# Performance work log

Measured on AMD Instinct MI355X. Metric: run time of the kernel, lower is better.

Reference implementation:

```python
import jax, jax.numpy as jnp
import numpy as np


def conv2d(x, w, b, pad):
    # x: [B,Cin,H,W], w: [Cout,Cin,kh,kw]
    y = jax.lax.conv_general_dilated(
        x, w, window_strides=(1, 1), padding=[(pad, pad), (pad, pad)],
        dimension_numbers=('NCHW', 'OIHW', 'NCHW'))
    return y + b[None, :, None, None]


def setup_inputs() -> dict:
    key = jax.random.key(0)
    ks = jax.random.split(key, 11)
    B, C, H, W = 4, 128, 64, 64
    Cc, Hc, Wc = 256, 32, 32
    s = 0.05
    return {
        'sr_feat': jax.random.normal(ks[0], (B, C, H, W), jnp.float32),
        'context_feat': jax.random.normal(ks[1], (B, Cc, Hc, Wc), jnp.float32),
        'Wq': jax.random.normal(ks[2], (C, C, 1, 1), jnp.float32) * s,
        'bq': jax.random.normal(ks[3], (C,), jnp.float32) * s,
        'Wk': jax.random.normal(ks[4], (C, Cc, 1, 1), jnp.float32) * s,
        'bk': jax.random.normal(ks[5], (C,), jnp.float32) * s,
        'Wv': jax.random.normal(ks[6], (C, Cc, 1, 1), jnp.float32) * s,
        'bv': jax.random.normal(ks[7], (C,), jnp.float32) * s,
        'Wp': jax.random.normal(ks[8], (C, C, 3, 3), jnp.float32) * s,
        'bp': jax.random.normal(ks[9], (C,), jnp.float32) * s,
        'gamma': jax.random.normal(ks[10], (1,), jnp.float32) * s,
    }


def reference(sr_feat, context_feat, Wq, bq, Wk, bk, Wv, bv, Wp, bp, gamma):
    B, C, H, W = sr_feat.shape
    Cc = context_feat.shape[1]
    # bilinear upsample (half-pixel centers == align_corners=False)
    ctx = jax.image.resize(context_feat, (B, Cc, H, W), method='bilinear')
    q = conv2d(sr_feat, Wq, bq, 0).reshape(B, C, H * W)   # [B,C,N]
    k = conv2d(ctx, Wk, bk, 0).reshape(B, C, H * W)       # [B,C,N]
    v = conv2d(ctx, Wv, bv, 0).reshape(B, C, H * W)       # [B,C,N]
    # attn[b,n,m] = softmax_m( sum_c q[b,c,n] * k[b,c,m] )
    attn = jax.nn.softmax(jnp.einsum('bcn,bcm->bnm', q, k), axis=-1)
    # out[b,c,n] = sum_m v[b,c,m] * attn[b,n,m]
    out = jnp.einsum('bcm,bnm->bcn', v, attn).reshape(B, C, H, W)
    return sr_feat + gamma[0] * conv2d(out, Wp, bp, 1)
```

## Files before the change

### kernel.cpp

```cpp
#include <hip/hip_runtime.h>
#include <math.h>

#define NB 4
#define C  128
#define CCH 256
#define HH 64
#define WW 64
#define NN 4096
#define NS 1024
#define HC 32
#define WC 32
#define PP 66
#define LOG2E 1.44269504088896f
#define NSPLIT 4

typedef unsigned short u16;
typedef unsigned int uint32;
typedef short s16x8 __attribute__((ext_vector_type(8)));
typedef float f32x4 __attribute__((ext_vector_type(4)));
typedef float f32x16 __attribute__((ext_vector_type(16)));

#if __has_builtin(__builtin_amdgcn_exp2f)
#define EXP2(x) __builtin_amdgcn_exp2f(x)
#else
#define EXP2(x) __expf((x) * 0.69314718056f)
#endif

__device__ __forceinline__ u16 f2bf(float f) {
    uint32 u = __float_as_uint(f);
    u += 0x7fffu + ((u >> 16) & 1u);
    return (u16)(u >> 16);
}
__device__ __forceinline__ float bf2f(u16 h) {
    return __uint_as_float((uint32)h << 16);
}

__global__ __launch_bounds__(256) void prep2(const float* __restrict__ ctx,
                                             const float* __restrict__ sr,
                                             const float* __restrict__ Wq,
                                             const float* __restrict__ Wk,
                                             const float* __restrict__ Wv,
                                             const float* __restrict__ Wp,
                                             u16* __restrict__ ctx_s,
                                             u16* __restrict__ sr_t,
                                             u16* __restrict__ wbf,
                                             u16* __restrict__ wt,
                                             uint4* __restrict__ att_z) {
    __shared__ float ls[64 * 65];
    int blk = blockIdx.x;
    int tid = threadIdx.x;

    if (blk < 256) {
        int idx = blk;
        int n0 = (idx & 15) * 64;
        int ci0 = ((idx >> 4) & 3) * 64;
        int b = idx >> 6;
        const float* inb = ctx + ((size_t)b * CCH + ci0) * NS + n0;
#pragma unroll
        for (int L = 0; L < 4; L++) {
            int fc = tid + L * 256;
            int nc = fc & 15, ci = fc >> 4;
            float4 v = *(const float4*)(inb + (size_t)ci * NS + nc * 4);
            float* d = &ls[ci * 65 + nc * 4];
            d[0] = v.x; d[1] = v.y; d[2] = v.z; d[3] = v.w;
        }
        __syncthreads();
        u16* ob = ctx_s + ((size_t)b * NS + n0) * CCH + ci0;
#pragma unroll
        for (int j = 0; j < 16; j++) {
            int o = tid + j * 256;
            int ci = o & 63, n = o >> 6;
            ob[(size_t)n * CCH + ci] = f2bf(ls[ci * 65 + n]);
        }
    } else if (blk < 768) {
        int idx = blk - 256;
        int n0 = (idx & 63) * 64;
        int ci0 = ((idx >> 6) & 1) * 64;
        int b = idx >> 7;
        const float* inb = sr + ((size_t)b * C + ci0) * NN + n0;
#pragma unroll
        for (int L = 0; L < 4; L++) {
            int fc = tid + L * 256;
            int nc = fc & 15, ci = fc >> 4;
            float4 v = *(const float4*)(inb + (size_t)ci * NN + nc * 4);
            float* d = &ls[ci * 65 + nc * 4];
            d[0] = v.x; d[1] = v.y; d[2] = v.z; d[3] = v.w;
        }
        __syncthreads();
        u16* ob = sr_t + ((size_t)b * NN + n0) * C + ci0;
#pragma unroll
        for (int j = 0; j < 16; j++) {
            int o = tid + j * 256;
            int ci = o & 63, n = o >> 6;
            ob[(size_t)n * C + ci] = f2bf(ls[ci * 65 + n]);
        }
    } else if (blk < 1664) {
        int i = (blk - 768) * 256 + tid;
        if (i < 81920) {
            float v;
            if (i < 16384) v = Wq[i] * LOG2E;
            else if (i < 49152) v = Wk[i - 16384];
            else v = Wv[i - 49152];
            wbf[i] = f2bf(v);
        } else {
            int idx = i - 81920;
            int ciin = idx & 31;
            int co = (idx >> 5) & 127;
            int cb = (idx >> 12) & 3;
            int pos = idx >> 14;
            int ky = pos / 3, kx = pos - ky * 3;
            int ci = cb * 32 + ciin;
            wt[idx] = f2bf(Wp[((size_t)(co * C + ci) * 3 + ky) * 3 + kx]);
        }
    } else {
        int i = (blk - 1664) * 256 + tid;
        if (i < 278784) att_z[i] = make_uint4(0, 0, 0, 0);
    }
}

__global__ __launch_bounds__(256) void proj_all2(const u16* __restrict__ sr_t,
                                                 const u16* __restrict__ ctx_s,
                                                 const u16* __restrict__ wbf,
                                                 const float* __restrict__ bq,
                                                 const float* __restrict__ bk,
                                                 const float* __restrict__ bv,
                                                 u16* __restrict__ q_t,
                                                 u16* __restrict__ k_s,
                                                 u16* __restrict__ v_s) {
    __shared__ u16 xs[128 * 64];
    __shared__ u16 wsm[2][128 * 64];
    int b = blockIdx.y;
    int tid = threadIdx.x;
    int w = tid >> 6, lane = tid & 63, l31 = lane & 31, half = lane >> 5;
    int xh = w >> 1, wh = w & 1;

    if (blockIdx.x < 32) {
        int n0 = blockIdx.x * 128;
        const u16* xb = sr_t + (size_t)b * NN * C;
        f32x16 acc[2][2];
#pragma unroll
        for (int xt = 0; xt < 2; xt++)
#pragma unroll
            for (int wt2 = 0; wt2 < 2; wt2++)
#pragma unroll
                for (int i = 0; i < 16; i++) acc[xt][wt2][i] = 0.f;
        for (int c0i = 0; c0i < 2; c0i++) {
            int c0 = c0i * 64;
            __syncthreads();
#pragma unroll
            for (int t = 0; t < 4; t++) {
                int CI = t * 256 + tid;
                int row = CI >> 3, sl = CI & 7;
                int lc = sl ^ (row & 7);
                __builtin_amdgcn_global_load_lds(
                    (const __attribute__((address_space(1))) void*)(xb + (size_t)(n0 + row) * C + c0 + lc * 8),
                    (__attribute__((address_space(3))) void*)&xs[(size_t)CI * 8], 16, 0, 0);
            }
#pragma unroll
            for (int t = 0; t < 4; t++) {
                int CI = t * 256 + tid;
                int co = CI >> 3, sl = CI & 7;
                int lc = sl ^ (co & 7);
                __builtin_amdgcn_global_load_lds(
                    (const __attribute__((address_space(1))) void*)(wbf + (size_t)co * C + c0 + lc * 8),
                    (__attribute__((address_space(3))) void*)&wsm[0][(size_t)CI * 8], 16, 0, 0);
            }
            __syncthreads();
#pragma unroll
            for (int kg = 0; kg < 4; kg++) {
                int pc = ((kg * 2 + half) ^ (l31 & 7)) * 8;
                s16x8 xf[2], wf2[2];
#pragma unroll
                for (int xt = 0; xt < 2; xt++)
                    xf[xt] = *(const s16x8*)&xs[(xh * 64 + xt * 32 + l31) * 64 + pc];
#pragma unroll
                for (int wt2 = 0; wt2 < 2; wt2++)
                    wf2[wt2] = *(const s16x8*)&wsm[0][(wh * 64 + wt2 * 32 + l31) * 64 + pc];
#pragma unroll
                for (int xt = 0; xt < 2; xt++)
#pragma unroll
                    for (int wt2 = 0; wt2 < 2; wt2++)
                        acc[xt][wt2] = __builtin_amdgcn_mfma_f32_32x32x16_bf16(xf[xt], wf2[wt2], acc[xt][wt2], 0, 0, 0);
            }
        }
        u16* ot = q_t + (size_t)b * NN * C;
        float bv2[2];
#pragma unroll
        for (int wt2 = 0; wt2 < 2; wt2++) bv2[wt2] = bq[wh * 64 + wt2 * 32 + l31] * LOG2E;
#pragma unroll
        for (int xt = 0; xt < 2; xt++)
#pragma unroll
            for (int r = 0; r < 16; r++) {
                int n = n0 + xh * 64 + xt * 32 + (r & 3) + 8 * (r >> 2) + 4 * half;
#pragma unroll
                for (int wt2 = 0; wt2 < 2; wt2++)
                    ot[(size_t)n * C + wh * 64 + wt2 * 32 + l31] = f2bf(acc[xt][wt2][r] + bv2[wt2]);
            }
    } else {
        int n0 = (blockIdx.x - 32) * 64;
        const u16* xb = ctx_s + (size_t)b * NS * CCH;
        const u16* wkb = wbf + 16384;
        const u16* wvb = wbf + 49152;
        f32x16 acck[2], accv[2];
#pragma unroll
        for (int wt2 = 0; wt2 < 2; wt2++)
#pragma unroll
            for (int i = 0; i < 16; i++) { acck[wt2][i] = 0.f; accv[wt2][i] = 0.f; }
        for (int c0i = 0; c0i < 4; c0i++) {
            int c0 = c0i * 64;
            __syncthreads();
#pragma unroll
            for (int t = 0; t < 2; t++) {
                int CI = t * 256 + tid;
                int row = CI >> 3, sl = CI & 7;
                int lc = sl ^ (row & 7);
                __builtin_amdgcn_global_load_lds(
                    (const __attribute__((address_space(1))) void*)(xb + (size_t)(n0 + row) * CCH + c0 + lc * 8),
                    (__attribute__((address_space(3))) void*)&xs[(size_t)CI * 8], 16, 0, 0);
            }
#pragma unroll
            for (int t = 0; t < 4; t++) {
                int CI = t * 256 + tid;
                int co = CI >> 3, sl = CI & 7;
                int lc = sl ^ (co & 7);
                __builtin_amdgcn_global_load_lds(
                    (const __attribute__((address_space(1))) void*)(wkb + (size_t)co * CCH + c0 + lc * 8),
                    (__attribute__((address_space(3))) void*)&wsm[0][(size_t)CI * 8], 16, 0, 0);
            }
#pragma unroll
            for (int t = 0; t < 4; t++) {
                int CI = t * 256 + tid;
                int co = CI >> 3, sl = CI & 7;
                int lc = sl ^ (co & 7);
                __builtin_amdgcn_global_load_lds(
                    (const __attribute__((address_space(1))) void*)(wvb + (size_t)co * CCH + c0 + lc * 8),
                    (__attribute__((address_space(3))) void*)&wsm[1][(size_t)CI * 8], 16, 0, 0);
            }
            __syncthreads();
#pragma unroll
            for (int kg = 0; kg < 4; kg++) {
                int pc = ((kg * 2 + half) ^ (l31 & 7)) * 8;
                s16x8 xf = *(const s16x8*)&xs[(xh * 32 + l31) * 64 + pc];
                s16x8 wfk[2], wfv[2];
#pragma unroll
                for (int wt2 = 0; wt2 < 2; wt2++) {
                    wfk[wt2] = *(const s16x8*)&wsm[0][(wh * 64 + wt2 * 32 + l31) * 64 + pc];
                    wfv[wt2] = *(const s16x8*)&wsm[1][(wh * 64 + wt2 * 32 + l31) * 64 + pc];
                }
#pragma unroll
                for (int wt2 = 0; wt2 < 2; wt2++) {
                    acck[wt2] = __builtin_amdgcn_mfma_f32_32x32x16_bf16(xf, wfk[wt2], acck[wt2], 0, 0, 0);
                    accv[wt2] = __builtin_amdgcn_mfma_f32_32x32x16_bf16(wfv[wt2], xf, accv[wt2], 0, 0, 0);
                }
            }
        }
        u16* ok = k_s + (size_t)b * NS * C;
#pragma unroll
        for (int wt2 = 0; wt2 < 2; wt2++) {
            float bvk = bk[wh * 64 + wt2 * 32 + l31];
#pragma unroll
            for (int r = 0; r < 16; r++) {
                int n = n0 + xh * 32 + (r & 3) + 8 * (r >> 2) + 4 * half;
                ok[(size_t)n * C + wh * 64 + wt2 * 32 + l31] = f2bf(acck[wt2][r] + bvk);
            }
        }
        u16* ov = v_s + (size_t)b * C * NS;
#pragma unroll
        for (int wt2 = 0; wt2 < 2; wt2++)
#pragma unroll
            for (int r = 0; r < 16; r++) {
                int co = wh * 64 + wt2 * 32 + (r & 3) + 8 * (r >> 2) + 4 * half;
                ov[(size_t)co * NS + n0 + xh * 32 + l31] = f2bf(accv[wt2][r] + bv[co]);
            }
    }
}

__global__ __launch_bounds__(256) void upsample_kv(const u16* __restrict__ k_s,
                                                   const u16* __restrict__ v_s,
                                                   u16* __restrict__ k_t,
                                                   u16* __restrict__ v_bf) {
    __shared__ u16 lsv[NS];
    int blk = blockIdx.x;
    int tid = threadIdx.x;
    if (blk < 256) {
        int y = blk & 63, b = blk >> 6;
        float sy = y * 0.5f - 0.25f;
        int y0 = (int)floorf(sy);
        float wy = sy - (float)y0;
        int y0c = y0 < 0 ? 0 : y0;
        int y1c = (y0 + 1 > HC - 1) ? HC - 1 : y0 + 1;
        int occ = tid & 127, xh = tid >> 7;
        const u16* kb = k_s + (size_t)b * NS * C;
        u16* ob = k_t + ((size_t)b * NN + (size_t)y * 64) * C + occ;
        float wy1 = 1.f - wy;
#pragma unroll
        for (int xi = 0; xi < 32; xi++) {
            int x = xi * 2 + xh;
            float sx = x * 0.5f - 0.25f;
            int x0 = (int)floorf(sx);
            float wx = sx - (float)x0;
            int x0c = x0 < 0 ? 0 : x0;
            int x1c = (x0 + 1 > WC - 1) ? WC - 1 : x0 + 1;
            float v00 = bf2f(kb[(size_t)(y0c * WC + x0c) * C + occ]);
            float v01 = bf2f(kb[(size_t)(y0c * WC + x1c) * C + occ]);
            float v10 = bf2f(kb[(size_t)(y1c * WC + x0c) * C + occ]);
            float v11 = bf2f(kb[(size_t)(y1c * WC + x1c) * C + occ]);
            float val = wy1 * ((1.f - wx) * v00 + wx * v01)
                      + wy  * ((1.f - wx) * v10 + wx * v11);
            ob[(size_t)x * C] = f2bf(val);
        }
    } else {
        int idx = blk - 256;
        int c = idx & 127, b = idx >> 7;
        const u16* vp = v_s + ((size_t)b * C + c) * NS;
        if (tid < 128) *(uint4*)&lsv[tid * 8] = *(const uint4*)(vp + tid * 8);
        __syncthreads();
        u16* ob = v_bf + ((size_t)b * C + c) * NN;
#pragma unroll
        for (int j = 0; j < 16; j++) {
            int n = tid + j * 256;
            int y = n >> 6, x = n & 63;
            float sy = y * 0.5f - 0.25f;
            float sx = x * 0.5f - 0.25f;
            int y0 = (int)floorf(sy), x0 = (int)floorf(sx);
            float wy = sy - (float)y0, wx = sx - (float)x0;
            int y0c = y0 < 0 ? 0 : y0;
            int y1c = (y0 + 1 > HC - 1) ? HC - 1 : y0 + 1;
            int x0c = x0 < 0 ? 0 : x0;
            int x1c = (x0 + 1 > WC - 1) ? WC - 1 : x0 + 1;
            float v00 = bf2f(lsv[y0c * WC + x0c]), v01 = bf2f(lsv[y0c * WC + x1c]);
            float v10 = bf2f(lsv[y1c * WC + x0c]), v11 = bf2f(lsv[y1c * WC + x1c]);
            ob[n] = f2bf((1.f - wy) * ((1.f - wx) * v00 + wx * v01)
                       +        wy  * ((1.f - wx) * v10 + wx * v11));
        }
    }
}

__global__ __launch_bounds__(256) void flash_mfma(const u16* __restrict__ qt_p,
                                                  const u16* __restrict__ kt_p,
                                                  const u16* __restrict__ vt_p,
                                                  u16* __restrict__ part,
                                                  float* __restrict__ lpart) {
    __shared__ u16 ks[2][64 * 128];
    __shared__ u16 vs[2][128 * 64];

    int ib = blockIdx.x;
    int b = (ib & 7) >> 1;
    int rest = ((ib >> 3) << 1) | (ib & 1);
    int qtile = rest >> 2;
    int split = rest & 3;
    int n0 = qtile * 128;
    int tid = threadIdx.x;
    int w = tid >> 6, lane = tid & 63, l31 = lane & 31, half = lane >> 5;

    const u16* qtb = qt_p + (size_t)b * NN * C;
    const u16* ktb = kt_p + (size_t)b * NN * C;
    const u16* vtb = vt_p + (size_t)b * C * NN;

    auto stageK = [&](int buf, int m0) {
#pragma unroll
        for (int t = 0; t < 4; t++) {
            int CI = (w * 4 + t) * 64 + lane;
            int r = CI >> 4;
            int lc = (CI & 15) ^ (r & 15);
            __builtin_amdgcn_global_load_lds(
                (const __attribute__((address_space(1))) void*)(ktb + (size_t)(m0 + r) * C + lc * 8),
                (__attribute__((address_space(3))) void*)&ks[buf][(w * 4 + t) * 512], 16, 0, 0);
        }
    };
    auto stageV = [&](int buf, int m0) {
#pragma unroll
        for (int t = 0; t < 4; t++) {
            int CI = (w * 4 + t) * 64 + lane;
            int c = CI >> 3;
            int lc = (CI & 7) ^ (c & 7);
            __builtin_amdgcn_global_load_lds(
                (const __attribute__((address_space(1))) void*)(vtb + (size_t)c * NN + m0 + lc * 8),
                (__attribute__((address_space(3))) void*)&vs[buf][(w * 4 + t) * 512], 16, 0, 0);
        }
    };

    int qrow = n0 + w * 32 + l31;
    s16x8 qf[8];
#pragma unroll
    for (int kg = 0; kg < 8; kg++)
        qf[kg] = *(const s16x8*)(qtb + (size_t)qrow * C + kg * 16 + half * 8);

    int m_base = split * 1024;
    stageK(0, m_base);
    stageV(0, m_base);
    __syncthreads();

    f32x16 oacc[4];
#pragma unroll
    for (int mt = 0; mt < 4; mt++)
#pragma unroll
        for (int i = 0; i < 16; i++) oacc[mt][i] = 0.f;
    float lsum = 0.f;

    for (int it = 0; it < 16; it++) {
        int buf = it & 1;
        int m0 = m_base + it * 64;
        if (it < 15) {
            stageK(buf ^ 1, m0 + 64);
            stageV(buf ^ 1, m0 + 64);
        }
        const u16* ksb = &ks[buf][0];
        const u16* vsb = &vs[buf][0];

#pragma unroll
        for (int kmt = 0; kmt < 2; kmt++) {
            f32x16 st;
#pragma unroll
            for (int i = 0; i < 16; i++) st[i] = 0.f;
#pragma unroll
            for (int kg = 0; kg < 8; kg++) {
                int pc = ((kg * 2 + half) ^ (l31 & 15)) * 8;
                s16x8 kf = *(const s16x8*)&ksb[(kmt * 32 + l31) * 128 + pc];
                st = __builtin_amdgcn_mfma_f32_32x32x16_bf16(kf, qf[kg], st, 0, 0, 0);
            }
            uint32 A[4], B4[4];
#pragma unroll
            for (int rg = 0; rg < 4; rg++) {
                float e0 = EXP2(st[rg * 4 + 0]);
                float e1 = EXP2(st[rg * 4 + 1]);
                float e2 = EXP2(st[rg * 4 + 2]);
                float e3 = EXP2(st[rg * 4 + 3]);
                lsum += (e0 + e1) + (e2 + e3);
                A[rg]  = __builtin_amdgcn_perm(__float_as_uint(e1), __float_as_uint(e0), 0x07060302u);
                B4[rg] = __builtin_amdgcn_perm(__float_as_uint(e3), __float_as_uint(e2), 0x07060302u);
            }
#pragma unroll
            for (int s = 0; s < 2; s++) {
                uint32 sendA = half ? A[2 * s] : A[2 * s + 1];
                uint32 sendB = half ? B4[2 * s] : B4[2 * s + 1];
                uint32 rA = __shfl_xor(sendA, 32);
                uint32 rB = __shfl_xor(sendB, 32);
                uint32 oA = half ? A[2 * s + 1] : A[2 * s];
                uint32 oB = half ? B4[2 * s + 1] : B4[2 * s];
                union { uint32 u[4]; s16x8 v; } pu;
                pu.u[0] = half ? rA : oA;
                pu.u[1] = half ? rB : oB;
                pu.u[2] = half ? oA : rA;
                pu.u[3] = half ? oB : rB;
                s16x8 pf = pu.v;
                int kgp = kmt * 2 + s;
                int pcv = ((kgp * 2 + half) ^ (l31 & 7)) * 8;
#pragma unroll
                for (int mt = 0; mt < 4; mt++) {
                    s16x8 vf = *(const s16x8*)&vsb[(mt * 32 + l31) * 64 + pcv];
                    oacc[mt] = __builtin_amdgcn_mfma_f32_32x32x16_bf16(vf, pf, oacc[mt], 0, 0, 0);
                }
            }
        }
        __syncthreads();
    }

    float lt = lsum + __shfl_xor(lsum, 32);
    if (half == 0) lpart[(size_t)split * NB * NN + (size_t)b * NN + qrow] = lt;
    u16* pb = part + ((size_t)split * NB + b) * (size_t)C * NN;
#pragma unroll
    for (int mt = 0; mt < 4; mt++)
#pragma unroll
        for (int r = 0; r < 16; r++) {
            int c = mt * 32 + (r & 3) + 8 * (r >> 2) + 4 * half;
            pb[(size_t)c * NN + n0 + w * 32 + l31] = f2bf(oacc[mt][r]);
        }
}

__global__ __launch_bounds__(256) void flash_combine(const u16* __restrict__ part,
                                                     const float* __restrict__ lpart,
                                                     u16* __restrict__ att_t) {
    __shared__ u16 ts[128 * 66];
    __shared__ float linv[64];
    int b = blockIdx.y;
    int nt = blockIdx.x;
    int n0 = nt * 64;
    int tid = threadIdx.x;
    if (tid < 64) {
        float s = 0.f;
#pragma unroll
        for (int sp = 0; sp < NSPLIT; sp++)
            s += lpart[(size_t)sp * NB * NN + (size_t)b * NN + n0 + tid];
        linv[tid] = 1.0f / s;
    }
    __syncthreads();
#pragma unroll
    for (int j = 0; j < 32; j++) {
        int e = tid + j * 256;
        int n = e & 63, c = e >> 6;
        float o = 0.f;
#pragma unroll
        for (int sp = 0; sp < NSPLIT; sp++)
            o += bf2f(part[((size_t)sp * NB + b) * (size_t)C * NN + (size_t)c * NN + n0 + n]);
        ts[c * 66 + n] = f2bf(o * linv[n]);
    }
    __syncthreads();
    u16* ob = att_t + ((size_t)b * PP * PP + (size_t)(nt + 1) * PP + 1) * C;
#pragma unroll
    for (int j = 0; j < 32; j++) {
        int o = tid + j * 256;
        int c = o & 127, n = o >> 7;
        ob[(size_t)n * C + c] = ts[c * 66 + n];
    }
}

__global__ __launch_bounds__(256) void conv3x3_mfma(const u16* __restrict__ att_t,
                                                    const u16* __restrict__ wt,
                                                    const float* __restrict__ bp,
                                                    const float* __restrict__ sr,
                                                    const float* __restrict__ gamma,
                                                    float* __restrict__ out) {
    __shared__ u16 in_s[2][4 * 102 * 8];
    int ib = blockIdx.x;
    int b = (ib & 7) >> 1;
    int rr = ((ib >> 3) << 1) | (ib & 1);
    int y = rr >> 1;
    int x0 = (rr & 1) * 32;
    int tid = threadIdx.x;
    int w = tid >> 6, lane = tid & 63, l = tid & 15, quad = (tid >> 4) & 3;
    const u16* ab = att_t + (size_t)b * (PP * PP * C);

    auto stage = [&](int cib, int bufi) {
        u16* base = &in_s[bufi][w * 102 * 8];
        const u16* gsrc = ab + cib * 32 + w * 8;
#pragma unroll
        for (int t = 0; t < 2; t++) {
            int idx = t * 64 + lane;
            int r = idx / 34, xp = idx - r * 34;
            if (t == 0 || lane < 38)
                __builtin_amdgcn_global_load_lds(
                    (const __attribute__((address_space(1))) void*)(gsrc + (size_t)((y + r) * PP + x0 + xp) * C),
                    (__attribute__((address_space(3))) void*)(base + (size_t)t * 64 * 8), 16, 0, 0);
        }
    };

    f32x4 accr[2][2];
#pragma unroll
    for (int cf = 0; cf < 2; cf++)
#pragma unroll
        for (int nf = 0; nf < 2; nf++) accr[cf][nf] = (f32x4){0.f, 0.f, 0.f, 0.f};
    int cow = w * 32;

    stage(0, 0);
    __syncthreads();
#pragma unroll
    for (int cib = 0; cib < 4; cib++) {
        if (cib < 3) stage(cib + 1, (cib + 1) & 1);
        s16x8 wf[9][2];
#pragma unroll
        for (int pos = 0; pos < 9; pos++)
#pragma unroll
            for (int cf = 0; cf < 2; cf++)
                wf[pos][cf] = *(const s16x8*)&wt[((size_t)(pos * 4 + cib) * C + cow + cf * 16 + l) * 32 + quad * 8];
        const u16* bufc = &in_s[cib & 1][0];
#pragma unroll
        for (int ky = 0; ky < 3; ky++)
#pragma unroll
            for (int kx = 0; kx < 3; kx++) {
                int pos = ky * 3 + kx;
#pragma unroll
                for (int nf = 0; nf < 2; nf++) {
                    s16x8 inf = *(const s16x8*)&bufc[(quad * 102 + ky * 34 + nf * 16 + l + kx) * 8];
                    accr[0][nf] = __builtin_amdgcn_mfma_f32_16x16x32_bf16(wf[pos][0], inf, accr[0][nf], 0, 0, 0);
                    accr[1][nf] = __builtin_amdgcn_mfma_f32_16x16x32_bf16(wf[pos][1], inf, accr[1][nf], 0, 0, 0);
                }
            }
        __syncthreads();
    }

    float g = gamma[0];
    float* ob = out + (size_t)b * C * NN;
    const float* sb = sr + (size_t)b * C * NN;
#pragma unroll
    for (int cf = 0; cf < 2; cf++)
#pragma unroll
        for (int r = 0; r < 4; r++) {
            int co = cow + cf * 16 + quad * 4 + r;
            float bias = bp[co];
#pragma unroll
            for (int nf = 0; nf < 2; nf++) {
                size_t oo = (size_t)co * NN + y * 64 + x0 + nf * 16 + l;
                ob[oo] = sb[oo] + g * (accr[cf][nf][r] + bias);
            }
        }
}

extern "C" void kernel_launch(void* const* d_in, const int* in_sizes, int n_in,
                              void* d_out, int out_size, void* d_ws, size_t ws_size,
                              hipStream_t stream) {
    const float* sr    = (const float*)d_in[0];
    const float* ctx   = (const float*)d_in[1];
    const float* Wq    = (const float*)d_in[2];
    const float* bq    = (const float*)d_in[3];
    const float* Wk    = (const float*)d_in[4];
    const float* bk    = (const float*)d_in[5];
    const float* Wv    = (const float*)d_in[6];
    const float* bv    = (const float*)d_in[7];
    const float* Wp    = (const float*)d_in[8];
    const float* bp    = (const float*)d_in[9];
    const float* gamma = (const float*)d_in[10];
    float* out = (float*)d_out;

    char* wsb = (char*)d_ws;
    u16*   att_t  = (u16*)wsb;
    u16*   part   = (u16*)(wsb + (5u << 20));
    float* lpart  = (float*)(wsb + (21u << 20));
    u16*   ctx_s  = (u16*)(wsb + (22u << 20));
    u16*   sr_t   = (u16*)(wsb + (25u << 20));
    u16*   q_t    = (u16*)(wsb + (29u << 20));
    u16*   k_s    = (u16*)(wsb + (33u << 20));
    u16*   v_s    = (u16*)(wsb + (34u << 20));
    u16*   k_t    = (u16*)(wsb + (35u << 20));
    u16*   v_bf   = (u16*)(wsb + (39u << 20));
    u16*   wt     = (u16*)(wsb + (43u << 20));
    u16*   w_bf   = (u16*)(wsb + (43u << 20) + (512u << 10));

    prep2<<<dim3(2753), 256, 0, stream>>>(ctx, sr, Wq, Wk, Wv, Wp,
                                          ctx_s, sr_t, w_bf, wt, (uint4*)att_t);
    proj_all2<<<dim3(48, NB), 256, 0, stream>>>(sr_t, ctx_s, w_bf, bq, bk, bv,
                                                q_t, k_s, v_s);
    upsample_kv<<<dim3(768), 256, 0, stream>>>(k_s, v_s, k_t, v_bf);
    flash_mfma<<<dim3(512), 256, 0, stream>>>(q_t, k_t, v_bf, part, lpart);
    flash_combine<<<dim3(64, NB), 256, 0, stream>>>(part, lpart, att_t);
    conv3x3_mfma<<<dim3(512), 256, 0, stream>>>(att_t, wt, bp, sr, gamma, out);
}
```

Before: 161.9 us.

## Compute attention scores on low-res keys and bilinearly interpolate scores

The separate upsampled K buffer is dropped. The flash kernel now computes QK scores against the 32x32 low-resolution keys and forms the upsampled-key scores by bilinearly interpolating those score tiles, which is valid because the 1x1 projection and interpolation are linear. This roughly halves the score MFMAs and removes the K-upsample pass and its global traffic. In exchange it adds cross-lane shuffles, a three-buffer K row pipeline with rolling score registers, and a launch_bounds occupancy hint.

```diff
diff --git a/kernel.cpp b/kernel.cpp
--- a/kernel.cpp
+++ b/kernel.cpp
@@ -275,73 +275,41 @@
     }
 }
 
-__global__ __launch_bounds__(256) void upsample_kv(const u16* __restrict__ k_s,
-                                                   const u16* __restrict__ v_s,
-                                                   u16* __restrict__ k_t,
-                                                   u16* __restrict__ v_bf) {
+__global__ __launch_bounds__(256) void upsample_v(const u16* __restrict__ v_s,
+                                                  u16* __restrict__ v_bf) {
     __shared__ u16 lsv[NS];
-    int blk = blockIdx.x;
+    int idx = blockIdx.x;
     int tid = threadIdx.x;
-    if (blk < 256) {
-        int y = blk & 63, b = blk >> 6;
+    int c = idx & 127, b = idx >> 7;
+    const u16* vp = v_s + ((size_t)b * C + c) * NS;
+    if (tid < 128) *(uint4*)&lsv[tid * 8] = *(const uint4*)(vp + tid * 8);
+    __syncthreads();
+    u16* ob = v_bf + ((size_t)b * C + c) * NN;
+#pragma unroll
+    for (int j = 0; j < 16; j++) {
+        int n = tid + j * 256;
+        int y = n >> 6, x = n & 63;
         float sy = y * 0.5f - 0.25f;
-        int y0 = (int)floorf(sy);
-        float wy = sy - (float)y0;
+        float sx = x * 0.5f - 0.25f;
+        int y0 = (int)floorf(sy), x0 = (int)floorf(sx);
+        float wy = sy - (float)y0, wx = sx - (float)x0;
         int y0c = y0 < 0 ? 0 : y0;
         int y1c = (y0 + 1 > HC - 1) ? HC - 1 : y0 + 1;
-        int occ = tid & 127, xh = tid >> 7;
-        const u16* kb = k_s + (size_t)b * NS * C;
-        u16* ob = k_t + ((size_t)b * NN + (size_t)y * 64) * C + occ;
-        float wy1 = 1.f - wy;
-#pragma unroll
-        for (int xi = 0; xi < 32; xi++) {
-            int x = xi * 2 + xh;
-            float sx = x * 0.5f - 0.25f;
-            int x0 = (int)floorf(sx);
-            float wx = sx - (float)x0;
-            int x0c = x0 < 0 ? 0 : x0;
-            int x1c = (x0 + 1 > WC - 1) ? WC - 1 : x0 + 1;
-            float v00 = bf2f(kb[(size_t)(y0c * WC + x0c) * C + occ]);
-            float v01 = bf2f(kb[(size_t)(y0c * WC + x1c) * C + occ]);
-            float v10 = bf2f(kb[(size_t)(y1c * WC + x0c) * C + occ]);
-            float v11 = bf2f(kb[(size_t)(y1c * WC + x1c) * C + occ]);
-            float val = wy1 * ((1.f - wx) * v00 + wx * v01)
-                      + wy  * ((1.f - wx) * v10 + wx * v11);
-            ob[(size_t)x * C] = f2bf(val);
-        }
-    } else {
-        int idx = blk - 256;
-        int c = idx & 127, b = idx >> 7;
-        const u16* vp = v_s + ((size_t)b * C + c) * NS;
-        if (tid < 128) *(uint4*)&lsv[tid * 8] = *(const uint4*)(vp + tid * 8);
-        __syncthreads();
-        u16* ob = v_bf + ((size_t)b * C + c) * NN;
-#pragma unroll
-        for (int j = 0; j < 16; j++) {
-            int n = tid + j * 256;
-            int y = n >> 6, x = n & 63;
-            float sy = y * 0.5f - 0.25f;
-            float sx = x * 0.5f - 0.25f;
-            int y0 = (int)floorf(sy), x0 = (int)floorf(sx);
-            float wy = sy - (float)y0, wx = sx - (float)x0;
-            int y0c = y0 < 0 ? 0 : y0;
-            int y1c = (y0 + 1 > HC - 1) ? HC - 1 : y0 + 1;
-            int x0c = x0 < 0 ? 0 : x0;
-            int x1c = (x0 + 1 > WC - 1) ? WC - 1 : x0 + 1;
-            float v00 = bf2f(lsv[y0c * WC + x0c]), v01 = bf2f(lsv[y0c * WC + x1c]);
-            float v10 = bf2f(lsv[y1c * WC + x0c]), v11 = bf2f(lsv[y1c * WC + x1c]);
-            ob[n] = f2bf((1.f - wy) * ((1.f - wx) * v00 + wx * v01)
-                       +        wy  * ((1.f - wx) * v10 + wx * v11));
-        }
-    }
-}
-
-__global__ __launch_bounds__(256) void flash_mfma(const u16* __restrict__ qt_p,
-                                                  const u16* __restrict__ kt_p,
-                                                  const u16* __restrict__ vt_p,
-                                                  u16* __restrict__ part,
-                                                  float* __restrict__ lpart) {
-    __shared__ u16 ks[2][64 * 128];
+        int x0c = x0 < 0 ? 0 : x0;
+        int x1c = (x0 + 1 > WC - 1) ? WC - 1 : x0 + 1;
+        float v00 = bf2f(lsv[y0c * WC + x0c]), v01 = bf2f(lsv[y0c * WC + x1c]);
+        float v10 = bf2f(lsv[y1c * WC + x0c]), v11 = bf2f(lsv[y1c * WC + x1c]);
+        ob[n] = f2bf((1.f - wy) * ((1.f - wx) * v00 + wx * v01)
+                   +        wy  * ((1.f - wx) * v10 + wx * v11));
+    }
+}
+
+__global__ __launch_bounds__(256, 2) void flash_mfma(const u16* __restrict__ qt_p,
+                                                     const u16* __restrict__ ks_p,
+                                                     const u16* __restrict__ vt_p,
+                                                     u16* __restrict__ part,
+                                                     float* __restrict__ lpart) {
+    __shared__ u16 ksr[3][32 * 128];
     __shared__ u16 vs[2][128 * 64];
 
     int ib = blockIdx.x;
@@ -354,18 +322,18 @@
     int w = tid >> 6, lane = tid & 63, l31 = lane & 31, half = lane >> 5;
 
     const u16* qtb = qt_p + (size_t)b * NN * C;
-    const u16* ktb = kt_p + (size_t)b * NN * C;
+    const u16* ksb = ks_p + (size_t)b * NS * C;
     const u16* vtb = vt_p + (size_t)b * C * NN;
 
-    auto stageK = [&](int buf, int m0) {
-#pragma unroll
-        for (int t = 0; t < 4; t++) {
-            int CI = (w * 4 + t) * 64 + lane;
-            int r = CI >> 4;
-            int lc = (CI & 15) ^ (r & 15);
+    auto stageKrow = [&](int buf, int r) {
+#pragma unroll
+        for (int t = 0; t < 2; t++) {
+            int CI = t * 256 + tid;
+            int row = CI >> 4;
+            int lc = (CI & 15) ^ (row & 15);
             __builtin_amdgcn_global_load_lds(
-                (const __attribute__((address_space(1))) void*)(ktb + (size_t)(m0 + r) * C + lc * 8),
-                (__attribute__((address_space(3))) void*)&ks[buf][(w * 4 + t) * 512], 16, 0, 0);
+                (const __attribute__((address_space(1))) void*)(ksb + (size_t)(r * 32 + row) * C + lc * 8),
+                (__attribute__((address_space(3))) void*)&ksr[buf][(size_t)CI * 8], 16, 0, 0);
         }
     };
     auto stageV = [&](int buf, int m0) {
@@ -386,10 +354,31 @@
     for (int kg = 0; kg < 8; kg++)
         qf[kg] = *(const s16x8*)(qtb + (size_t)qrow * C + kg * 16 + half * 8);
 
+    auto scoreTile = [&](int buf) {
+        f32x16 st;
+#pragma unroll
+        for (int i = 0; i < 16; i++) st[i] = 0.f;
+        const u16* kb = &ksr[buf][0];
+#pragma unroll
+        for (int kg = 0; kg < 8; kg++) {
+            int pc = ((kg * 2 + half) ^ (l31 & 15)) * 8;
+            s16x8 kf = *(const s16x8*)&kb[l31 * 128 + pc];
+            st = __builtin_amdgcn_mfma_f32_32x32x16_bf16(kf, qf[kg], st, 0, 0, 0);
+        }
+        return st;
+    };
+
     int m_base = split * 1024;
-    stageK(0, m_base);
+    int j0 = split * 8;
+
+    stageKrow(0, split == 0 ? 0 : j0 - 1);
+    stageKrow(1, j0);
+    stageKrow(2, j0 + 1);
     stageV(0, m_base);
     __syncthreads();
+    f32x16 sA = scoreTile(0);
+    f32x16 sB = scoreTile(1);
+    f32x16 sC;
 
     f32x16 oacc[4];
 #pragma unroll
@@ -398,59 +387,75 @@
         for (int i = 0; i < 16; i++) oacc[mt][i] = 0.f;
     float lsum = 0.f;
 
+#pragma unroll 2
     for (int it = 0; it < 16; it++) {
         int buf = it & 1;
         int m0 = m_base + it * 64;
         if (it < 15) {
-            stageK(buf ^ 1, m0 + 64);
             stageV(buf ^ 1, m0 + 64);
-        }
-        const u16* ksb = &ks[buf][0];
+            if (it & 1) {
+                int rs = j0 + 2 + (it >> 1);
+                if (rs <= 31) stageKrow((it >> 1) % 3, rs);
+            }
+        }
+        if (!(it & 1)) {
+            int rn = j0 + 1 + (it >> 1);
+            if (rn <= 31) sC = scoreTile((2 + (it >> 1)) % 3);
+        } else {
+            sA = sB;
+            int rn = j0 + 1 + (it >> 1);
+            if (rn <= 31) sB = sC;
+        }
+
+        float wB = (it & 1) ? 0.25f : 0.75f;
+        float wA = 1.0f - wB;
+        float cc[16];
+#pragma unroll
+        for (int i = 0; i < 16; i++) cc[i] = wA * sA[i] + wB * sB[i];
+
+        float xr0  = __shfl_xor(cc[0], 32);
+        float xr3  = __shfl_xor(cc[3], 32);
+        float xr4  = __shfl_xor(cc[4], 32);
+        float xr7  = __shfl_xor(cc[7], 32);
+        float xr8  = __shfl_xor(cc[8], 32);
+        float xr11 = __shfl_xor(cc[11], 32);
+        float xr12 = __shfl_xor(cc[12], 32);
+        float xr15 = __shfl_xor(cc[15], 32);
+        float d0s[4], d5s[4];
+        d0s[0] = half ? xr3  : cc[0];
+        d0s[1] = half ? xr7  : xr3;
+        d0s[2] = half ? xr11 : xr7;
+        d0s[3] = half ? xr15 : xr11;
+        d5s[0] = half ? xr4  : xr0;
+        d5s[1] = half ? xr8  : xr4;
+        d5s[2] = half ? xr12 : xr8;
+        d5s[3] = half ? cc[15] : xr12;
+
         const u16* vsb = &vs[buf][0];
-
-#pragma unroll
-        for (int kmt = 0; kmt < 2; kmt++) {
-            f32x16 st;
-#pragma unroll
-            for (int i = 0; i < 16; i++) st[i] = 0.f;
-#pragma unroll
-            for (int kg = 0; kg < 8; kg++) {
-                int pc = ((kg * 2 + half) ^ (l31 & 15)) * 8;
-                s16x8 kf = *(const s16x8*)&ksb[(kmt * 32 + l31) * 128 + pc];
-                st = __builtin_amdgcn_mfma_f32_32x32x16_bf16(kf, qf[kg], st, 0, 0, 0);
-            }
-            uint32 A[4], B4[4];
-#pragma unroll
-            for (int rg = 0; rg < 4; rg++) {
-                float e0 = EXP2(st[rg * 4 + 0]);
-                float e1 = EXP2(st[rg * 4 + 1]);
-                float e2 = EXP2(st[rg * 4 + 2]);
-                float e3 = EXP2(st[rg * 4 + 3]);
-                lsum += (e0 + e1) + (e2 + e3);
-                A[rg]  = __builtin_amdgcn_perm(__float_as_uint(e1), __float_as_uint(e0), 0x07060302u);
-                B4[rg] = __builtin_amdgcn_perm(__float_as_uint(e3), __float_as_uint(e2), 0x07060302u);
-            }
-#pragma unroll
-            for (int s = 0; s < 2; s++) {
-                uint32 sendA = half ? A[2 * s] : A[2 * s + 1];
-                uint32 sendB = half ? B4[2 * s] : B4[2 * s + 1];
-                uint32 rA = __shfl_xor(sendA, 32);
-                uint32 rB = __shfl_xor(sendB, 32);
-                uint32 oA = half ? A[2 * s + 1] : A[2 * s];
-                uint32 oB = half ? B4[2 * s + 1] : B4[2 * s];
-                union { uint32 u[4]; s16x8 v; } pu;
-                pu.u[0] = half ? rA : oA;
-                pu.u[1] = half ? rB : oB;
-                pu.u[2] = half ? oA : rA;
-                pu.u[3] = half ? oB : rB;
-                s16x8 pf = pu.v;
-                int kgp = kmt * 2 + s;
-                int pcv = ((kgp * 2 + half) ^ (l31 & 7)) * 8;
-#pragma unroll
-                for (int mt = 0; mt < 4; mt++) {
-                    s16x8 vf = *(const s16x8*)&vsb[(mt * 32 + l31) * 64 + pcv];
-                    oacc[mt] = __builtin_amdgcn_mfma_f32_32x32x16_bf16(vf, pf, oacc[mt], 0, 0, 0);
-                }
+#pragma unroll
+        for (int s = 0; s < 4; s++) {
+            float d0 = d0s[s], d1 = cc[4 * s], d2 = cc[4 * s + 1];
+            float d3 = cc[4 * s + 2], d4 = cc[4 * s + 3], d5 = d5s[s];
+            float e1 = 0.75f * d1, e2 = 0.75f * d2, e3 = 0.75f * d3, e4 = 0.75f * d4;
+            float p0 = EXP2(fmaf(0.25f, d0, e1));
+            float p1 = EXP2(fmaf(0.25f, d2, e1));
+            float p2 = EXP2(fmaf(0.25f, d1, e2));
+            float p3 = EXP2(fmaf(0.25f, d3, e2));
+            float p4 = EXP2(fmaf(0.25f, d2, e3));
+            float p5 = EXP2(fmaf(0.25f, d4, e3));
+            float p6 = EXP2(fmaf(0.25f, d3, e4));
+            float p7 = EXP2(fmaf(0.25f, d5, e4));
+            lsum += ((p0 + p1) + (p2 + p3)) + ((p4 + p5) + (p6 + p7));
+            union { uint32 u[4]; s16x8 v; } pu;
+            pu.u[0] = __builtin_amdgcn_perm(__float_as_uint(p1), __float_as_uint(p0), 0x07060302u);
+            pu.u[1] = __builtin_amdgcn_perm(__float_as_uint(p3), __float_as_uint(p2), 0x07060302u);
+            pu.u[2] = __builtin_amdgcn_perm(__float_as_uint(p5), __float_as_uint(p4), 0x07060302u);
+            pu.u[3] = __builtin_amdgcn_perm(__float_as_uint(p7), __float_as_uint(p6), 0x07060302u);
+            int pcv = ((s * 2 + half) ^ (l31 & 7)) * 8;
+#pragma unroll
+            for (int mt = 0; mt < 4; mt++) {
+                s16x8 vf = *(const s16x8*)&vsb[(mt * 32 + l31) * 64 + pcv];
+                oacc[mt] = __builtin_amdgcn_mfma_f32_32x32x16_bf16(vf, pu.v, oacc[mt], 0, 0, 0);
             }
         }
         __syncthreads();
@@ -611,7 +616,6 @@
     u16*   q_t    = (u16*)(wsb + (29u << 20));
     u16*   k_s    = (u16*)(wsb + (33u << 20));
     u16*   v_s    = (u16*)(wsb + (34u << 20));
-    u16*   k_t    = (u16*)(wsb + (35u << 20));
     u16*   v_bf   = (u16*)(wsb + (39u << 20));
     u16*   wt     = (u16*)(wsb + (43u << 20));
     u16*   w_bf   = (u16*)(wsb + (43u << 20) + (512u << 10));
@@ -620,8 +624,8 @@
                                           ctx_s, sr_t, w_bf, wt, (uint4*)att_t);
     proj_all2<<<dim3(48, NB), 256, 0, stream>>>(sr_t, ctx_s, w_bf, bq, bk, bv,
                                                 q_t, k_s, v_s);
-    upsample_kv<<<dim3(768), 256, 0, stream>>>(k_s, v_s, k_t, v_bf);
-    flash_mfma<<<dim3(512), 256, 0, stream>>>(q_t, k_t, v_bf, part, lpart);
+    upsample_v<<<dim3(512), 256, 0, stream>>>(v_s, v_bf);
+    flash_mfma<<<dim3(512), 256, 0, stream>>>(q_t, k_s, v_bf, part, lpart);
     flash_combine<<<dim3(64, NB), 256, 0, stream>>>(part, lpart, att_t);
     conv3x3_mfma<<<dim3(512), 256, 0, stream>>>(att_t, wt, bp, sr, gamma, out);
 }
```

New measurement: 150.2 us. -7.2%, faster.
